# Optimization experiments

Hardware: AMD Instinct MI355X
Metric: run time of the kernel (lower is better)

## Reference

```python
import jax, jax.numpy as jnp
import numpy as np

VOCAB, DIM = 100000, 512
BATCH, SEQ = 4096, 200
HID, OUT = 256, 20


def setup_inputs() -> dict:
    key = jax.random.key(0)
    k_emb, k_x, k_len, k_w1, k_b1, k_w2, k_b2 = jax.random.split(key, 7)
    emb_table = jax.random.normal(k_emb, (VOCAB, DIM), dtype=jnp.float32) * 0.1
    x = jax.random.randint(k_x, (BATCH, SEQ), 0, VOCAB, dtype=jnp.int64)
    # lengths in [1, SEQ] to avoid division by zero, matching real padded batches
    lengths = jax.random.randint(k_len, (BATCH,), 1, SEQ + 1, dtype=jnp.int64)
    bows = jnp.zeros((BATCH,), dtype=jnp.float32)  # unused by the model's forward
    # Linear(2*DIM, 256) and Linear(256, OUT); stored transposed for x @ W
    W1 = jax.random.normal(k_w1, (2 * DIM, HID), dtype=jnp.float32) * (1.0 / np.sqrt(2 * DIM))
    b1 = jax.random.normal(k_b1, (HID,), dtype=jnp.float32) * 0.01
    W2 = jax.random.normal(k_w2, (HID, OUT), dtype=jnp.float32) * (1.0 / np.sqrt(HID))
    b2 = jax.random.normal(k_b2, (OUT,), dtype=jnp.float32) * 0.01
    return {"emb_table": emb_table, "W1": W1, "b1": b1, "W2": W2, "b2": b2,
            "x": x, "lengths": lengths, "bows": bows}


def reference(emb_table, W1, b1, W2, b2, x, lengths, bows):
    # Gather: [B, S, D]
    emb = emb_table[x]
    # Faithful to original: sum over the FULL sequence (padding included),
    # divided by the true length; max also over the full sequence.
    rep_mean = jnp.sum(emb, axis=1) / lengths.astype(emb.dtype)[:, None]  # [B, D]
    rep_max = jnp.max(emb, axis=1)                                        # [B, D]
    rep = jnp.concatenate([rep_mean, rep_max], axis=1)                    # [B, 2D]
    h = jax.nn.relu(rep @ W1 + b1)                                        # [B, 256]
    logits = h @ W2 + b2                                                  # [B, OUT]
    return logits
```

## Files before the change

### kernel.cpp

```cpp
#include <hip/hip_runtime.h>
#include <hip/hip_bf16.h>

#define VOCAB 100000
#define DIM   512
#define BATCH 4096
#define SEQ   200
#define HID   256
#define OUTN  20

typedef __attribute__((ext_vector_type(8))) short short8;
typedef __attribute__((ext_vector_type(4))) float floatx4;

static __device__ __forceinline__ unsigned short f2bf(float f) {
    __hip_bfloat16 b = __float2bfloat16(f);
    return *(unsigned short*)&b;
}
static __device__ __forceinline__ float bf2f(unsigned short u) {
    unsigned int v = (unsigned int)u << 16;
    return *(float*)&v;
}

__global__ __launch_bounds__(256) void k_cvt(
    const float* __restrict__ src, unsigned short* __restrict__ dst)
{
    const int n8 = VOCAB * DIM / 8;
    int i = blockIdx.x * 256 + threadIdx.x;
    const int stride = gridDim.x * 256;
    const floatx4* s4 = (const floatx4*)src;
    short8* d8 = (short8*)dst;
    for (; i < n8; i += stride) {
        const floatx4 a = __builtin_nontemporal_load(&s4[2 * i]);
        const floatx4 b = __builtin_nontemporal_load(&s4[2 * i + 1]);
        short8 o;
        o[0] = (short)f2bf(a[0]); o[1] = (short)f2bf(a[1]);
        o[2] = (short)f2bf(a[2]); o[3] = (short)f2bf(a[3]);
        o[4] = (short)f2bf(b[0]); o[5] = (short)f2bf(b[1]);
        o[6] = (short)f2bf(b[2]); o[7] = (short)f2bf(b[3]);
        d8[i] = o;
    }
}

__global__ __launch_bounds__(256) void k_reduce_bf(
    const unsigned short* __restrict__ embb, const int* __restrict__ x,
    const int* __restrict__ lengths, unsigned short* __restrict__ repb)
{
    const int b = blockIdx.x;
    const int t = threadIdx.x;
    const int w = t >> 6;
    const int lane = t & 63;

    __shared__ int sidx[SEQ];
    for (int i = t; i < SEQ; i += 256) sidx[i] = x[b * SEQ + i];
    __syncthreads();

    float s[8] = {0.f, 0.f, 0.f, 0.f, 0.f, 0.f, 0.f, 0.f};
    float m[8] = {-1e30f, -1e30f, -1e30f, -1e30f, -1e30f, -1e30f, -1e30f, -1e30f};

    const unsigned short* base = embb + lane * 8;
    const int i0 = w * (SEQ / 4);

#pragma unroll 5
    for (int i = i0; i < i0 + SEQ / 4; ++i) {
        const short8 v = *(const short8*)(base + (size_t)sidx[i] * DIM);
#pragma unroll
        for (int j = 0; j < 8; ++j) {
            const float f = bf2f((unsigned short)v[j]);
            s[j] += f;
            m[j] = fmaxf(m[j], f);
        }
    }

    __shared__ float red[4][2][DIM];
#pragma unroll
    for (int j = 0; j < 8; ++j) {
        red[w][0][lane * 8 + j] = s[j];
        red[w][1][lane * 8 + j] = m[j];
    }
    __syncthreads();

    const float inv = 1.0f / (float)lengths[b];
    const int c0 = t * 2;
    unsigned int mu = 0, xu = 0;
#pragma unroll
    for (int j = 0; j < 2; ++j) {
        const float sv = red[0][0][c0 + j] + red[1][0][c0 + j]
                       + red[2][0][c0 + j] + red[3][0][c0 + j];
        const float mv = fmaxf(fmaxf(red[0][1][c0 + j], red[1][1][c0 + j]),
                               fmaxf(red[2][1][c0 + j], red[3][1][c0 + j]));
        mu |= (unsigned int)f2bf(sv * inv) << (16 * j);
        xu |= (unsigned int)f2bf(mv)       << (16 * j);
    }
    unsigned short* row = repb + (size_t)b * (2 * DIM);
    *(unsigned int*)(row + c0)       = mu;
    *(unsigned int*)(row + DIM + c0) = xu;
}

__global__ __launch_bounds__(128) void k_reduce(
    const float* __restrict__ emb, const int* __restrict__ x,
    const int* __restrict__ lengths, unsigned short* __restrict__ repb)
{
    const int b = blockIdx.x;
    const int t = threadIdx.x;

    __shared__ int sidx[SEQ];
    for (int i = t; i < SEQ; i += 128) sidx[i] = x[b * SEQ + i];
    __syncthreads();

    const float4* embv = (const float4*)emb;
    float4 s = make_float4(0.f, 0.f, 0.f, 0.f);
    float4 m = make_float4(-1e30f, -1e30f, -1e30f, -1e30f);

#pragma unroll 4
    for (int i = 0; i < SEQ; ++i) {
        const float4 v = embv[(size_t)sidx[i] * (DIM / 4) + t];
        s.x += v.x; s.y += v.y; s.z += v.z; s.w += v.w;
        m.x = fmaxf(m.x, v.x); m.y = fmaxf(m.y, v.y);
        m.z = fmaxf(m.z, v.z); m.w = fmaxf(m.w, v.w);
    }

    const float inv = 1.0f / (float)lengths[b];
    unsigned long long mu =
          (unsigned long long)f2bf(s.x * inv)
        | ((unsigned long long)f2bf(s.y * inv) << 16)
        | ((unsigned long long)f2bf(s.z * inv) << 32)
        | ((unsigned long long)f2bf(s.w * inv) << 48);
    unsigned long long xu =
          (unsigned long long)f2bf(m.x)
        | ((unsigned long long)f2bf(m.y) << 16)
        | ((unsigned long long)f2bf(m.z) << 32)
        | ((unsigned long long)f2bf(m.w) << 48);

    unsigned short* row = repb + (size_t)b * (2 * DIM);
    *(unsigned long long*)(row + 4 * t)       = mu;
    *(unsigned long long*)(row + DIM + 4 * t) = xu;
}

__global__ __launch_bounds__(256) void k_w1t(
    const float* __restrict__ W1, unsigned short* __restrict__ W1T)
{
    __shared__ unsigned short s[64][65];
    const int n0 = blockIdx.x * 64;
    const int k0 = blockIdx.y * 64;
    const int t = threadIdx.x;

#pragma unroll
    for (int i = 0; i < 4; ++i) {
        const int kk = (t >> 4) + i * 16;
        const int cc = (t & 15) * 4;
        const float4 v = *(const float4*)&W1[(size_t)(k0 + kk) * HID + n0 + cc];
        s[cc + 0][kk] = f2bf(v.x);
        s[cc + 1][kk] = f2bf(v.y);
        s[cc + 2][kk] = f2bf(v.z);
        s[cc + 3][kk] = f2bf(v.w);
    }
    __syncthreads();

#pragma unroll
    for (int i = 0; i < 4; ++i) {
        const int nn = (t >> 4) + i * 16;
        const int kq = (t & 15) * 4;
        unsigned long long u =
              (unsigned long long)s[nn][kq + 0]
            | ((unsigned long long)s[nn][kq + 1] << 16)
            | ((unsigned long long)s[nn][kq + 2] << 32)
            | ((unsigned long long)s[nn][kq + 3] << 48);
        *(unsigned long long*)&W1T[(size_t)(n0 + nn) * (2 * DIM) + k0 + kq] = u;
    }
}

#define APAD 40

__global__ __launch_bounds__(256) void k_gemm1(
    const unsigned short* __restrict__ repb,
    const unsigned short* __restrict__ w1t,
    const float* __restrict__ bias, float* __restrict__ h)
{
    const int K = 2 * DIM;
    const int rowBase = blockIdx.y * 64;
    const int colBase = blockIdx.x * 64;
    const int tid  = threadIdx.x;
    const int lane = tid & 63;
    const int wv   = tid >> 6;
    const int wm   = wv & 1;
    const int wn   = wv >> 1;

    __shared__ unsigned short sA[64][APAD];
    __shared__ unsigned short sB[64][APAD];

    const int r  = tid >> 2;
    const int kq = tid & 3;

    const unsigned short* gA = repb + (size_t)(rowBase + r) * K + kq * 8;
    const unsigned short* gB = w1t  + (size_t)(colBase + r) * K + kq * 8;

    floatx4 acc[2][2] = {{{0.f,0.f,0.f,0.f},{0.f,0.f,0.f,0.f}},
                         {{0.f,0.f,0.f,0.f},{0.f,0.f,0.f,0.f}}};

    short8 pa = *(const short8*)gA;
    short8 pb = *(const short8*)gB;

    const int lm = lane & 15;
    const int lq = lane >> 4;
    for (int k0 = 0; k0 < K; k0 += 32) {
        __syncthreads();
        *(short8*)&sA[r][kq * 8] = pa;
        *(short8*)&sB[r][kq * 8] = pb;
        __syncthreads();

        if (k0 + 32 < K) {
            pa = *(const short8*)(gA + k0 + 32);
            pb = *(const short8*)(gB + k0 + 32);
        }

        const short8 a0 = *(const short8*)&sA[wm * 32 + lm][lq * 8];
        const short8 a1 = *(const short8*)&sA[wm * 32 + 16 + lm][lq * 8];
        const short8 b0 = *(const short8*)&sB[wn * 32 + lm][lq * 8];
        const short8 b1 = *(const short8*)&sB[wn * 32 + 16 + lm][lq * 8];

        acc[0][0] = __builtin_amdgcn_mfma_f32_16x16x32_bf16(a0, b0, acc[0][0], 0, 0, 0);
        acc[0][1] = __builtin_amdgcn_mfma_f32_16x16x32_bf16(a0, b1, acc[0][1], 0, 0, 0);
        acc[1][0] = __builtin_amdgcn_mfma_f32_16x16x32_bf16(a1, b0, acc[1][0], 0, 0, 0);
        acc[1][1] = __builtin_amdgcn_mfma_f32_16x16x32_bf16(a1, b1, acc[1][1], 0, 0, 0);
    }

#pragma unroll
    for (int nt = 0; nt < 2; ++nt) {
        const int col = colBase + wn * 32 + nt * 16 + lm;
        const float bb = bias[col];
#pragma unroll
        for (int mt = 0; mt < 2; ++mt) {
#pragma unroll
            for (int rg = 0; rg < 4; ++rg) {
                const int row = rowBase + wm * 32 + mt * 16 + lq * 4 + rg;
                h[(size_t)row * HID + col] = fmaxf(acc[mt][nt][rg] + bb, 0.f);
            }
        }
    }
}

#define R3 32
#define HP4 260

__global__ __launch_bounds__(256) void k_gemm2(
    const float* __restrict__ H, const float* __restrict__ W2,
    const float* __restrict__ b2, float* __restrict__ outp)
{
    __shared__ float sh[R3][HP4];
    __shared__ float swt[OUTN][HP4];
    __shared__ float sb[OUTN];

    const int t = threadIdx.x;
    const int rowBase = blockIdx.x * R3;

    const float4* H4 = (const float4*)H;
    for (int i = t; i < R3 * (HID / 4); i += 256) {
        const int r  = i >> 6;
        const int c4 = i & 63;
        *(float4*)&sh[r][c4 * 4] = H4[(size_t)(rowBase + r) * (HID / 4) + c4];
    }
    {
        const int k = t;
#pragma unroll
        for (int c = 0; c < OUTN; ++c) swt[c][k] = W2[k * OUTN + c];
    }
    if (t < OUTN) sb[t] = b2[t];
    __syncthreads();

    const int r  = t & 31;
    const int cs = t >> 5;
    float a0 = sb[cs], a1 = sb[cs + 8], a2 = (cs + 16 < OUTN) ? sb[cs + 16] : 0.f;
    float acc0 = 0.f, acc1 = 0.f, acc2 = 0.f;

#pragma unroll 8
    for (int k = 0; k < HID; k += 4) {
        const float4 a = *(const float4*)&sh[r][k];
        const float4 w0 = *(const float4*)&swt[cs][k];
        const float4 w1 = *(const float4*)&swt[cs + 8][k];
        acc0 += a.x * w0.x + a.y * w0.y + a.z * w0.z + a.w * w0.w;
        acc1 += a.x * w1.x + a.y * w1.y + a.z * w1.z + a.w * w1.w;
        if (cs + 16 < OUTN) {
            const float4 w2 = *(const float4*)&swt[cs + 16][k];
            acc2 += a.x * w2.x + a.y * w2.y + a.z * w2.z + a.w * w2.w;
        }
    }

    float* orow = outp + (size_t)(rowBase + r) * OUTN;
    orow[cs]     = acc0 + a0;
    orow[cs + 8] = acc1 + a1;
    if (cs + 16 < OUTN) orow[cs + 16] = acc2 + a2;
}

extern "C" void kernel_launch(void* const* d_in, const int* in_sizes, int n_in,
                              void* d_out, int out_size, void* d_ws, size_t ws_size,
                              hipStream_t stream)
{
    const float* emb     = (const float*)d_in[0];
    const float* W1      = (const float*)d_in[1];
    const float* b1      = (const float*)d_in[2];
    const float* W2      = (const float*)d_in[3];
    const float* b2      = (const float*)d_in[4];
    const int*   x       = (const int*)d_in[5];
    const int*   lengths = (const int*)d_in[6];

    float* out = (float*)d_out;

    const size_t embbN = (size_t)VOCAB * DIM;
    const size_t repbN = (size_t)BATCH * 2 * DIM;
    const size_t w1tN  = (size_t)HID * 2 * DIM;
    const size_t hN    = (size_t)BATCH * HID;
    const size_t needFast = (embbN + repbN + w1tN) * 2 + hN * 4 + 256;

    if (ws_size >= needFast) {
        unsigned short* embb = (unsigned short*)d_ws;
        unsigned short* repb = embb + embbN;
        unsigned short* w1t  = repb + repbN;
        float* h = (float*)(w1t + w1tN);

        k_cvt<<<2048, 256, 0, stream>>>(emb, embb);
        k_w1t<<<dim3(HID / 64, (2 * DIM) / 64), 256, 0, stream>>>(W1, w1t);
        k_reduce_bf<<<BATCH, 256, 0, stream>>>(embb, x, lengths, repb);
        k_gemm1<<<dim3(HID / 64, BATCH / 64), 256, 0, stream>>>(repb, w1t, b1, h);
        k_gemm2<<<BATCH / R3, 256, 0, stream>>>(h, W2, b2, out);
    } else {
        unsigned short* repb = (unsigned short*)d_ws;
        unsigned short* w1t  = repb + repbN;
        float* h = (float*)(w1t + w1tN);

        k_w1t<<<dim3(HID / 64, (2 * DIM) / 64), 256, 0, stream>>>(W1, w1t);
        k_reduce<<<BATCH, 128, 0, stream>>>(emb, x, lengths, repb);
        k_gemm1<<<dim3(HID / 64, BATCH / 64), 256, 0, stream>>>(repb, w1t, b1, h);
        k_gemm2<<<BATCH / R3, 256, 0, stream>>>(h, W2, b2, out);
    }
}
```

Before: 424.9 us.

## Fuse both MLP GEMMs into one kernel keeping hidden activations in LDS

Replaces the separate first-layer MFMA GEMM and second-layer GEMM kernels with a single kernel. Each block handles 16 batch rows across all 256 hidden units, keeps the ReLU output in shared memory, and computes the 20 logits directly. This removes the global write and read of the hidden matrix and one launch. In exchange, each block re-reads the full transposed W1 (now 256 blocks doing so), and there are fewer waves per block doing MFMA work.

```diff
diff --git a/kernel.cpp b/kernel.cpp
--- a/kernel.cpp
+++ b/kernel.cpp
@@ -168,126 +168,95 @@
     }
 }
 
-#define APAD 40
-
-__global__ __launch_bounds__(256) void k_gemm1(
+#define MB 16
+#define KPAD 36
+
+__global__ __launch_bounds__(256) void k_mlp(
     const unsigned short* __restrict__ repb,
     const unsigned short* __restrict__ w1t,
-    const float* __restrict__ bias, float* __restrict__ h)
+    const float* __restrict__ b1,
+    const float* __restrict__ W2,
+    const float* __restrict__ b2,
+    float* __restrict__ outp)
 {
     const int K = 2 * DIM;
-    const int rowBase = blockIdx.y * 64;
-    const int colBase = blockIdx.x * 64;
+    const int rowBase = blockIdx.x * MB;
     const int tid  = threadIdx.x;
     const int lane = tid & 63;
     const int wv   = tid >> 6;
-    const int wm   = wv & 1;
-    const int wn   = wv >> 1;
-
-    __shared__ unsigned short sA[64][APAD];
-    __shared__ unsigned short sB[64][APAD];
-
-    const int r  = tid >> 2;
-    const int kq = tid & 3;
-
-    const unsigned short* gA = repb + (size_t)(rowBase + r) * K + kq * 8;
-    const unsigned short* gB = w1t  + (size_t)(colBase + r) * K + kq * 8;
-
-    floatx4 acc[2][2] = {{{0.f,0.f,0.f,0.f},{0.f,0.f,0.f,0.f}},
-                         {{0.f,0.f,0.f,0.f},{0.f,0.f,0.f,0.f}}};
-
-    short8 pa = *(const short8*)gA;
-    short8 pb = *(const short8*)gB;
+
+    __shared__ unsigned short sA[MB][KPAD];
+    __shared__ unsigned short sB[HID][KPAD];
+    __shared__ float sh[MB][HID + 4];
+    __shared__ float swt[OUTN][HID + 4];
+    __shared__ float sb2[OUTN];
+
+    for (int i = tid; i < HID * OUTN; i += 256) {
+        const int k = i / OUTN, c = i - k * OUTN;
+        swt[c][k] = W2[i];
+    }
+    if (tid < OUTN) sb2[tid] = b2[tid];
+
+    const int ar  = tid >> 2;
+    const int akq = tid & 3;
+    const bool aldr = (tid < 64);
+    const unsigned short* gA = repb + (size_t)(rowBase + (aldr ? ar : 0)) * K + akq * 8;
+    const short8* gB = (const short8*)(w1t + (size_t)tid * K);
+
+    floatx4 acc[4] = {{0.f,0.f,0.f,0.f},{0.f,0.f,0.f,0.f},
+                      {0.f,0.f,0.f,0.f},{0.f,0.f,0.f,0.f}};
+
+    short8 pa = aldr ? *(const short8*)gA : short8{};
+    short8 pb0 = gB[0], pb1 = gB[1], pb2 = gB[2], pb3 = gB[3];
 
     const int lm = lane & 15;
     const int lq = lane >> 4;
     for (int k0 = 0; k0 < K; k0 += 32) {
         __syncthreads();
-        *(short8*)&sA[r][kq * 8] = pa;
-        *(short8*)&sB[r][kq * 8] = pb;
+        if (aldr) *(short8*)&sA[ar][akq * 8] = pa;
+        *(short8*)&sB[tid][0]  = pb0;
+        *(short8*)&sB[tid][8]  = pb1;
+        *(short8*)&sB[tid][16] = pb2;
+        *(short8*)&sB[tid][24] = pb3;
         __syncthreads();
 
         if (k0 + 32 < K) {
-            pa = *(const short8*)(gA + k0 + 32);
-            pb = *(const short8*)(gB + k0 + 32);
-        }
-
-        const short8 a0 = *(const short8*)&sA[wm * 32 + lm][lq * 8];
-        const short8 a1 = *(const short8*)&sA[wm * 32 + 16 + lm][lq * 8];
-        const short8 b0 = *(const short8*)&sB[wn * 32 + lm][lq * 8];
-        const short8 b1 = *(const short8*)&sB[wn * 32 + 16 + lm][lq * 8];
-
-        acc[0][0] = __builtin_amdgcn_mfma_f32_16x16x32_bf16(a0, b0, acc[0][0], 0, 0, 0);
-        acc[0][1] = __builtin_amdgcn_mfma_f32_16x16x32_bf16(a0, b1, acc[0][1], 0, 0, 0);
-        acc[1][0] = __builtin_amdgcn_mfma_f32_16x16x32_bf16(a1, b0, acc[1][0], 0, 0, 0);
-        acc[1][1] = __builtin_amdgcn_mfma_f32_16x16x32_bf16(a1, b1, acc[1][1], 0, 0, 0);
-    }
-
-#pragma unroll
-    for (int nt = 0; nt < 2; ++nt) {
-        const int col = colBase + wn * 32 + nt * 16 + lm;
-        const float bb = bias[col];
-#pragma unroll
-        for (int mt = 0; mt < 2; ++mt) {
-#pragma unroll
-            for (int rg = 0; rg < 4; ++rg) {
-                const int row = rowBase + wm * 32 + mt * 16 + lq * 4 + rg;
-                h[(size_t)row * HID + col] = fmaxf(acc[mt][nt][rg] + bb, 0.f);
-            }
-        }
-    }
-}
-
-#define R3 32
-#define HP4 260
-
-__global__ __launch_bounds__(256) void k_gemm2(
-    const float* __restrict__ H, const float* __restrict__ W2,
-    const float* __restrict__ b2, float* __restrict__ outp)
-{
-    __shared__ float sh[R3][HP4];
-    __shared__ float swt[OUTN][HP4];
-    __shared__ float sb[OUTN];
-
-    const int t = threadIdx.x;
-    const int rowBase = blockIdx.x * R3;
-
-    const float4* H4 = (const float4*)H;
-    for (int i = t; i < R3 * (HID / 4); i += 256) {
-        const int r  = i >> 6;
-        const int c4 = i & 63;
-        *(float4*)&sh[r][c4 * 4] = H4[(size_t)(rowBase + r) * (HID / 4) + c4];
-    }
-    {
-        const int k = t;
-#pragma unroll
-        for (int c = 0; c < OUTN; ++c) swt[c][k] = W2[k * OUTN + c];
-    }
-    if (t < OUTN) sb[t] = b2[t];
-    __syncthreads();
-
-    const int r  = t & 31;
-    const int cs = t >> 5;
-    float a0 = sb[cs], a1 = sb[cs + 8], a2 = (cs + 16 < OUTN) ? sb[cs + 16] : 0.f;
-    float acc0 = 0.f, acc1 = 0.f, acc2 = 0.f;
-
+            if (aldr) pa = *(const short8*)(gA + k0 + 32);
+            const int g = (k0 + 32) >> 3;
+            pb0 = gB[g]; pb1 = gB[g + 1]; pb2 = gB[g + 2]; pb3 = gB[g + 3];
+        }
+
+        const short8 a = *(const short8*)&sA[lm][lq * 8];
+#pragma unroll
+        for (int nt = 0; nt < 4; ++nt) {
+            const short8 bfrag = *(const short8*)&sB[wv * 64 + nt * 16 + lm][lq * 8];
+            acc[nt] = __builtin_amdgcn_mfma_f32_16x16x32_bf16(a, bfrag, acc[nt], 0, 0, 0);
+        }
+    }
+
+#pragma unroll
+    for (int nt = 0; nt < 4; ++nt) {
+        const int col = wv * 64 + nt * 16 + lm;
+        const float bb = b1[col];
+#pragma unroll
+        for (int rg = 0; rg < 4; ++rg)
+            sh[lq * 4 + rg][col] = fmaxf(acc[nt][rg] + bb, 0.f);
+    }
+    __syncthreads();
+
+#pragma unroll
+    for (int o = tid; o < MB * OUTN; o += 256) {
+        const int r = o / OUTN;
+        const int c = o - r * OUTN;
+        float a0 = sb2[c];
 #pragma unroll 8
-    for (int k = 0; k < HID; k += 4) {
-        const float4 a = *(const float4*)&sh[r][k];
-        const float4 w0 = *(const float4*)&swt[cs][k];
-        const float4 w1 = *(const float4*)&swt[cs + 8][k];
-        acc0 += a.x * w0.x + a.y * w0.y + a.z * w0.z + a.w * w0.w;
-        acc1 += a.x * w1.x + a.y * w1.y + a.z * w1.z + a.w * w1.w;
-        if (cs + 16 < OUTN) {
-            const float4 w2 = *(const float4*)&swt[cs + 16][k];
-            acc2 += a.x * w2.x + a.y * w2.y + a.z * w2.z + a.w * w2.w;
-        }
-    }
-
-    float* orow = outp + (size_t)(rowBase + r) * OUTN;
-    orow[cs]     = acc0 + a0;
-    orow[cs + 8] = acc1 + a1;
-    if (cs + 16 < OUTN) orow[cs + 16] = acc2 + a2;
+        for (int k = 0; k < HID; k += 4) {
+            const float4 hv = *(const float4*)&sh[r][k];
+            const float4 wvv = *(const float4*)&swt[c][k];
+            a0 += hv.x * wvv.x + hv.y * wvv.y + hv.z * wvv.z + hv.w * wvv.w;
+        }
+        outp[(size_t)(rowBase + r) * OUTN + c] = a0;
+    }
 }
 
 extern "C" void kernel_launch(void* const* d_in, const int* in_sizes, int n_in,
@@ -307,28 +276,23 @@
     const size_t embbN = (size_t)VOCAB * DIM;
     const size_t repbN = (size_t)BATCH * 2 * DIM;
     const size_t w1tN  = (size_t)HID * 2 * DIM;
-    const size_t hN    = (size_t)BATCH * HID;
-    const size_t needFast = (embbN + repbN + w1tN) * 2 + hN * 4 + 256;
+    const size_t needFast = (embbN + repbN + w1tN) * 2 + 256;
 
     if (ws_size >= needFast) {
         unsigned short* embb = (unsigned short*)d_ws;
         unsigned short* repb = embb + embbN;
         unsigned short* w1t  = repb + repbN;
-        float* h = (float*)(w1t + w1tN);
 
         k_cvt<<<2048, 256, 0, stream>>>(emb, embb);
         k_w1t<<<dim3(HID / 64, (2 * DIM) / 64), 256, 0, stream>>>(W1, w1t);
         k_reduce_bf<<<BATCH, 256, 0, stream>>>(embb, x, lengths, repb);
-        k_gemm1<<<dim3(HID / 64, BATCH / 64), 256, 0, stream>>>(repb, w1t, b1, h);
-        k_gemm2<<<BATCH / R3, 256, 0, stream>>>(h, W2, b2, out);
+        k_mlp<<<BATCH / MB, 256, 0, stream>>>(repb, w1t, b1, W2, b2, out);
     } else {
         unsigned short* repb = (unsigned short*)d_ws;
         unsigned short* w1t  = repb + repbN;
-        float* h = (float*)(w1t + w1tN);
 
         k_w1t<<<dim3(HID / 64, (2 * DIM) / 64), 256, 0, stream>>>(W1, w1t);
         k_reduce<<<BATCH, 128, 0, stream>>>(emb, x, lengths, repb);
-        k_gemm1<<<dim3(HID / 64, BATCH / 64), 256, 0, stream>>>(repb, w1t, b1, h);
-        k_gemm2<<<BATCH / R3, 256, 0, stream>>>(h, W2, b2, out);
-    }
-}
+        k_mlp<<<BATCH / MB, 256, 0, stream>>>(repb, w1t, b1, W2, b2, out);
+    }
+}
```

Result: no change. 431.8 us (+1.6%).
